# Performance work log

Measured on AMD Instinct MI355X. Metric: run time of the kernel, lower is better.

## Reference

```python
import jax, jax.numpy as jnp
import numpy as np

BL = 512  # block length (matches init bl)


def _conv1x1(w, b, x):
    # w: (out, in), b: (out,), x: (batch, in, L) -> (batch, out, L)
    return jnp.einsum('oi,bil->bol', w, x) + b[None, :, None]


def _window_mask(bl):
    # Faithful to torch loop: window_mask[:, :, i:i+bl] = 1 for i in range(bl)
    # -> all ones except the last column.
    wm = np.zeros((1, bl, bl + 2 * (bl // 2)), np.float32)
    for i in range(bl):
        wm[:, :, i:i + bl] = 1.0
    return jnp.asarray(wm)


def setup_inputs() -> dict:
    key = jax.random.key(0)
    ks = jax.random.split(key, 5)
    B, C, L = 1, 2048, 16384
    Cq = C // 2  # r1 = r2 = r3 = 2
    s_in = 1.0 / float(np.sqrt(C))
    s_mid = 1.0 / float(np.sqrt(Cq))
    return {
        'x1': jax.random.normal(ks[0], (B, C, L), jnp.float32),
        'x2': jnp.zeros((B, C, L), jnp.float32),
        'mask': jnp.ones((B, 1, L), jnp.float32),
        'wq': jax.random.normal(ks[1], (Cq, C), jnp.float32) * s_in,
        'bq': jnp.zeros((Cq,), jnp.float32),
        'wk': jax.random.normal(ks[2], (Cq, C), jnp.float32) * s_in,
        'bk': jnp.zeros((Cq,), jnp.float32),
        'wv': jax.random.normal(ks[3], (Cq, C), jnp.float32) * s_in,
        'bv': jnp.zeros((Cq,), jnp.float32),
        'wo': jax.random.normal(ks[4], (C, Cq), jnp.float32) * s_mid,
        'bo': jnp.zeros((C,), jnp.float32),
    }


def reference(x1, x2, mask, wq, bq, wk, bk, wv, bv, wo, bo):
    B, C, L = x1.shape  # B == 1 (asserted by sliding path)
    bl = BL
    nb = L // bl  # L % bl == 0 by construction
    half = bl // 2

    q = _conv1x1(wq, bq, x1)  # (1, c, L)
    k = _conv1x1(wk, bk, x1)
    v = _conv1x1(wv, bv, x1)  # encoder stage: value from x1 (x2 unused)
    c = q.shape[1]

    # query blocks: (nb, c, bl)
    qb = q.reshape(B, c, nb, bl).transpose(0, 2, 1, 3).reshape(nb, c, bl)

    # pad k/v/padding_mask with bl//2 zeros on both sides, then take overlapping
    # windows of width 2*bl per block.
    kp = jnp.pad(k, ((0, 0), (0, 0), (half, half)))[0]            # (c, L+bl)
    vp = jnp.pad(v, ((0, 0), (0, 0), (half, half)))[0]
    pm = jnp.pad(mask[:, 0:1, :], ((0, 0), (0, 0), (half, half)))[0]  # (1, L+bl)
    cols = np.arange(nb)[:, None] * bl + np.arange(2 * bl)[None, :]   # (nb, 2bl)
    kb = kp[:, cols].transpose(1, 0, 2)   # (nb, c, 2bl)
    vb = vp[:, cols].transpose(1, 0, 2)   # (nb, c, 2bl)
    pmb = pm[:, cols].transpose(1, 0, 2)  # (nb, 1, 2bl)

    final_mask = _window_mask(bl) * pmb   # (nb, bl, 2bl)

    # scalar dot attention with log-mask (as in AttentionHelper.scalar_dot_att)
    energy = jnp.einsum('ncl,ncm->nlm', qb, kb) / jnp.float32(np.sqrt(c))
    attn = jax.nn.softmax(energy + jnp.log(final_mask + 1e-9), axis=-1)
    attn = attn * final_mask
    out = jnp.einsum('ncm,nlm->ncl', vb, attn)  # (nb, c, bl)

    out = _conv1x1(wo, bo, jax.nn.relu(out))    # (nb, C, bl)
    out = out.reshape(B, nb, C, bl).transpose(0, 2, 1, 3).reshape(B, C, nb * bl)
    out = out[:, :, :L]
    return out * mask[:, 0:1, :]
```

## Files before the change

kernel.cpp:

```cpp
#include <hip/hip_runtime.h>
#include <hip/hip_bf16.h>

typedef __attribute__((ext_vector_type(4))) float f32x4;
typedef __attribute__((ext_vector_type(8))) __bf16 bf16x8;

struct ushort4_t { unsigned short x, y, z, w; };

#define DEVINL static __device__ __forceinline__

DEVINL unsigned short f2bf(float f) {
  union { float f; unsigned u; } x; x.f = f;
  return (unsigned short)((x.u + 0x7FFFu + ((x.u >> 16) & 1u)) >> 16);
}

DEVINL void gload16(const void* g, void* l) {
  __builtin_amdgcn_global_load_lds((const __attribute__((address_space(1))) void*)g,
                                   (__attribute__((address_space(3))) void*)l,
                                   16, 0, 0);
}

#define SBAR()   asm volatile("s_barrier" ::: "memory")
#define LGKM(n)  asm volatile("s_waitcnt lgkmcnt(" #n ")" ::: "memory")
#define VM(n)    asm volatile("s_waitcnt vmcnt(" #n ")" ::: "memory")
#define SCHED0() __builtin_amdgcn_sched_barrier(0)

__global__ __launch_bounds__(256) void transpose_x_k(const float* __restrict__ x,
                                                     unsigned short* __restrict__ xT) {
  __shared__ float tile[32][33];
  const int bx = blockIdx.x;
  const int by = blockIdx.y;
  const int tx = threadIdx.x;
  const int ty = threadIdx.y;
#pragma unroll
  for (int i = 0; i < 4; ++i) {
    int c = by * 32 + ty + i * 8;
    tile[ty + i * 8][tx] = x[(long)c * 16384 + bx * 32 + tx];
  }
  __syncthreads();
  const int t = ty * 32 + tx;
  const int lrow = t >> 3;
  const int cq = (t & 7) << 2;
  ushort4_t o;
  o.x = f2bf(tile[cq + 0][lrow]);
  o.y = f2bf(tile[cq + 1][lrow]);
  o.z = f2bf(tile[cq + 2][lrow]);
  o.w = f2bf(tile[cq + 3][lrow]);
  *reinterpret_cast<ushort4_t*>(xT + (long)(bx * 32 + lrow) * 2048 + by * 32 + cq) = o;
}

__global__ __launch_bounds__(256) void conv_w_k(const float* __restrict__ wq,
                                                const float* __restrict__ wk,
                                                const float* __restrict__ wv,
                                                const float* __restrict__ wo,
                                                unsigned short* __restrict__ Wqk,
                                                unsigned short* __restrict__ Wv,
                                                unsigned short* __restrict__ Wo) {
  long i = ((long)blockIdx.x * 256 + threadIdx.x) * 4;
  const float* src;
  unsigned short* dst;
  if (i < 4194304) {
    src = (i < 2097152) ? (wq + i) : (wk + i - 2097152);
    dst = Wqk + i;
  } else if (i < 6291456) {
    src = wv + (i - 4194304);
    dst = Wv + (i - 4194304);
  } else {
    src = wo + (i - 6291456);
    dst = Wo + (i - 6291456);
  }
  float4 v = *reinterpret_cast<const float4*>(src);
  ushort4_t o{f2bf(v.x), f2bf(v.y), f2bf(v.z), f2bf(v.w)};
  *reinterpret_cast<ushort4_t*>(dst) = o;
}

enum { EPI_QK = 0, EPI_V = 1, EPI_S = 2, EPI_PV = 3, EPI_OUT = 4 };

struct GArgs {
  const unsigned short* A;
  const unsigned short* Bt;
  void* C;
  const float* bias;
  const float* bias2;
  const float* mask;
  const unsigned short* guard;
  int aBatch, cBatch;
  int btRow0, btRow0Step, btRowLim;
  int btK0, btK0Step, btKLim;
};

template <int EPI, int GUARDED, int LDA, int LDB, int LDC, int KK>
__global__ __launch_bounds__(512, 2) void gemm8_k(GArgs g) {
  constexpr int NK = KK >> 6;
  __shared__ char lds[131072];

  const int t = threadIdx.x;
  const int l = t & 63;
  const int w = t >> 6;

  const int gx = gridDim.x, gxy = gx * gridDim.y;
  const int nwg = gxy * gridDim.z;
  int lin = blockIdx.z * gxy + blockIdx.y * gx + blockIdx.x;
  lin = (lin & 7) * (nwg >> 3) + (lin >> 3);
  const int z = lin / gxy;
  const int rres = lin - z * gxy;
  const int Mbase = (rres / gx) << 8;
  const int Nbase = (rres - (rres / gx) * gx) << 8;

  const int wr = w >> 2;
  const int wc = w & 3;
  const int fr = l & 15;
  const int fg = l >> 4;

  const unsigned short* Ab = g.A + (long)z * g.aBatch + (long)Mbase * LDA;
  const int bRowBase = g.btRow0 + z * g.btRow0Step + Nbase;
  const int bK0 = g.btK0 + z * g.btK0Step;

  const int rr = t >> 3;
  const int cb8s = t & 7;

  auto stage = [&](int bufSel, int unit, int kt) {
    const int k0 = (kt & (NK - 1)) << 6;
    const bool isA = (unit == 0) || (unit == 3);
#pragma unroll
    for (int gph = 0; gph < 2; ++gph) {
      int row;
      if (isA) row = (unit == 0 ? 0 : 64) + (gph << 7) + rr;
      else     row = (unit == 1 ? 0 : 32) + (gph << 7) + (rr & 31) + ((rr >> 5) << 6);
      const int cbL = cb8s ^ (row & 7);
      const int gk = k0 + (cbL << 3);
      char* lp = lds + (bufSel << 16) + (isA ? 0 : 32768) + row * 128 + (cb8s << 4);
      const char* gp;
      if (isA) {
        gp = (const char*)(Ab + (long)row * LDA + gk);
      } else if (!GUARDED) {
        gp = (const char*)(g.Bt + (long)(bRowBase + row) * LDB + (bK0 + gk));
      } else {
        const int grow = bRowBase + row;
        const int gkk = bK0 + gk;
        if ((unsigned)grow < (unsigned)g.btRowLim && (unsigned)gkk < (unsigned)g.btKLim)
          gp = (const char*)(g.Bt + (long)grow * LDB + gkk);
        else
          gp = (const char*)g.guard + (l << 4);
      }
      gload16(gp, lp);
    }
  };

  const int arow = (wr << 7) + fr;
  const int brow = (wc << 6) + fr;

  auto ldA = [&](int i8, int kk, int bufSel) -> bf16x8 {
    const int row = arow + (i8 << 4);
    const int cb = ((kk << 2) | fg) ^ (row & 7);
    return *(const bf16x8*)(lds + (bufSel << 16) + row * 128 + (cb << 4));
  };
  auto ldB = [&](int j, int kk, int bufSel) -> bf16x8 {
    const int row = brow + (j << 4);
    const int cb = ((kk << 2) | fg) ^ (row & 7);
    return *(const bf16x8*)(lds + (bufSel << 16) + 32768 + row * 128 + (cb << 4));
  };

  f32x4 acc[8][4];
#pragma unroll
  for (int i = 0; i < 8; ++i)
#pragma unroll
    for (int j = 0; j < 4; ++j) acc[i][j] = f32x4{0.f, 0.f, 0.f, 0.f};

  bf16x8 fa[4][2], fb[4][2];

#define MFMA_Q(QI, QJ)                                                        \
  __builtin_amdgcn_s_setprio(1);                                              \
  _Pragma("unroll") for (int kk = 0; kk < 2; ++kk)                            \
  _Pragma("unroll") for (int i = 0; i < 4; ++i)                               \
  _Pragma("unroll") for (int j = 0; j < 2; ++j)                               \
    acc[(QI)*4 + i][(QJ)*2 + j] = __builtin_amdgcn_mfma_f32_16x16x32_bf16(    \
        fa[i][kk], fb[(QJ)*2 + j][kk], acc[(QI)*4 + i][(QJ)*2 + j], 0, 0, 0); \
  __builtin_amdgcn_s_setprio(0);

  stage(0, 0, 0); stage(0, 1, 0); stage(0, 2, 0); stage(0, 3, 0);
  stage(1, 0, 1); stage(1, 1, 1); stage(1, 2, 1); stage(1, 3, 1);
  VM(8);
  SBAR();

#pragma unroll 1
  for (int kt = 0; kt < NK; ++kt) {
    const int cur = kt & 1;
    const int ktn = kt + 2;
#pragma unroll
    for (int i = 0; i < 4; ++i) { fa[i][0] = ldA(i, 0, cur); fa[i][1] = ldA(i, 1, cur); }
#pragma unroll
    for (int j = 0; j < 2; ++j) { fb[j][0] = ldB(j, 0, cur); fb[j][1] = ldB(j, 1, cur); }
    SCHED0();
#pragma unroll
    for (int j = 2; j < 4; ++j) { fb[j][0] = ldB(j, 0, cur); fb[j][1] = ldB(j, 1, cur); }
    LGKM(4); SCHED0();
    MFMA_Q(0, 0);
    SBAR();
    stage(cur, 0, ktn); stage(cur, 1, ktn);
    LGKM(0); SCHED0();
    MFMA_Q(0, 1);
#pragma unroll
    for (int i = 0; i < 4; ++i) { fa[i][0] = ldA(4 + i, 0, cur); fa[i][1] = ldA(4 + i, 1, cur); }
    LGKM(0); SCHED0();
    MFMA_Q(1, 0);
    SBAR();
    stage(cur, 2, ktn); stage(cur, 3, ktn);
    MFMA_Q(1, 1);
    VM(8); SBAR();
  }
  VM(0); LGKM(0); SBAR();

#pragma unroll
  for (int ii = 0; ii < 8; ++ii)
#pragma unroll
    for (int j = 0; j < 4; ++j)
#pragma unroll
      for (int r = 0; r < 4; ++r) {
        const int row = Mbase + (wr << 7) + ii * 16 + fg * 4 + r;
        const int col = Nbase + (wc << 6) + j * 16 + fr;
        float val = acc[ii][j][r];
        const long off = (long)z * g.cBatch + (long)row * LDC + col;
        if (EPI == EPI_QK) {
          val = (col < 1024) ? (val + g.bias[col]) * 0.03125f
                             : (val + g.bias2[col - 1024]);
          ((unsigned short*)g.C)[off] = f2bf(val);
        } else if (EPI == EPI_V) {
          val += g.bias[row];
          ((unsigned short*)g.C)[off] = f2bf(val);
        } else if (EPI == EPI_S) {
          ((float*)g.C)[off] = val;
        } else if (EPI == EPI_PV) {
          val = fmaxf(val, 0.f);
          ((unsigned short*)g.C)[off] = f2bf(val);
        } else {
          val = (val + g.bias[row]) * g.mask[col];
          ((float*)g.C)[off] = val;
        }
      }
#undef MFMA_Q
}

__global__ __launch_bounds__(256) void softmax_k(const float* __restrict__ S,
                                                 const float* __restrict__ mask,
                                                 unsigned short* __restrict__ P) {
  const int row = blockIdx.x;
  const int n = row >> 9;
  const float* s = S + (long)row * 1024;
  unsigned short* p = P + (long)row * 1024;
  const int t = threadIdx.x;

  const float4 sv = *reinterpret_cast<const float4*>(s + t * 4);
  const int pos0 = (n << 9) + t * 4 - 256;
  float4 mv = {0.f, 0.f, 0.f, 0.f};
  if ((unsigned)pos0 < 16384u) mv = *reinterpret_cast<const float4*>(mask + pos0);
  float fm[4] = {mv.x, mv.y, mv.z, mv.w};
  if (t == 255) fm[3] = 0.f;
  const float sc[4] = {sv.x, sv.y, sv.z, sv.w};

  float logit[4];
  float lmax = -3.0e38f;
#pragma unroll
  for (int k = 0; k < 4; ++k) {
    logit[k] = sc[k] + logf(fm[k] + 1e-9f);
    lmax = fmaxf(lmax, logit[k]);
  }
#pragma unroll
  for (int o = 32; o; o >>= 1) lmax = fmaxf(lmax, __shfl_xor(lmax, o, 64));
  __shared__ float red[8];
  const int wv_ = t >> 6, ln = t & 63;
  if (ln == 0) red[wv_] = lmax;
  __syncthreads();
  const float gmax = fmaxf(fmaxf(red[0], red[1]), fmaxf(red[2], red[3]));

  float e[4], lsum = 0.f;
#pragma unroll
  for (int k = 0; k < 4; ++k) { e[k] = expf(logit[k] - gmax); lsum += e[k]; }
#pragma unroll
  for (int o = 32; o; o >>= 1) lsum += __shfl_xor(lsum, o, 64);
  if (ln == 0) red[4 + wv_] = lsum;
  __syncthreads();
  const float inv = 1.f / ((red[4] + red[5]) + (red[6] + red[7]));
  ushort4_t o4;
  o4.x = f2bf(e[0] * inv * fm[0]);
  o4.y = f2bf(e[1] * inv * fm[1]);
  o4.z = f2bf(e[2] * inv * fm[2]);
  o4.w = f2bf(e[3] * inv * fm[3]);
  *reinterpret_cast<ushort4_t*>(p + t * 4) = o4;
}

extern "C" void kernel_launch(void* const* d_in, const int* in_sizes, int n_in,
                              void* d_out, int out_size, void* d_ws, size_t ws_size,
                              hipStream_t stream) {
  const float* x1 = (const float*)d_in[0];
  const float* mask = (const float*)d_in[2];
  const float* wq = (const float*)d_in[3];
  const float* bq = (const float*)d_in[4];
  const float* wk = (const float*)d_in[5];
  const float* bk = (const float*)d_in[6];
  const float* wv = (const float*)d_in[7];
  const float* bv = (const float*)d_in[8];
  const float* wo = (const float*)d_in[9];
  const float* bo = (const float*)d_in[10];

  char* ws = (char*)d_ws;
  unsigned short* xT   = (unsigned short*)(ws);
  unsigned short* attT = xT;
  unsigned short* Wqk  = (unsigned short*)(ws + 67108864);
  unsigned short* Wv   = (unsigned short*)(ws + 75497472);
  unsigned short* Wo   = (unsigned short*)(ws + 79691776);
  unsigned short* qkT  = (unsigned short*)(ws + 83886080);
  unsigned short* vbuf = (unsigned short*)(ws + 150994944);
  float*          Sbuf = (float*)(ws + 184549376);
  unsigned short* P    = (unsigned short*)(ws + 251658240);
  unsigned short* guard= (unsigned short*)(ws + 285212672);

  hipMemsetAsync(guard, 0, 4096, stream);

  transpose_x_k<<<dim3(512, 64), dim3(32, 8), 0, stream>>>(x1, xT);
  conv_w_k<<<dim3(8192), dim3(256), 0, stream>>>(wq, wk, wv, wo, Wqk, Wv, Wo);

  const int BIG = 0x40000000;
  {
    GArgs a{};
    a.A = xT; a.Bt = Wqk; a.C = qkT;
    a.bias = bq; a.bias2 = bk; a.guard = guard;
    a.aBatch = 0; a.cBatch = 0;
    a.btRow0 = 0; a.btRow0Step = 0; a.btRowLim = BIG;
    a.btK0 = 0; a.btK0Step = 0; a.btKLim = BIG;
    gemm8_k<EPI_QK, 0, 2048, 2048, 2048, 2048><<<dim3(8, 64, 1), 512, 0, stream>>>(a);
  }
  {
    GArgs a{};
    a.A = Wv; a.Bt = xT; a.C = vbuf;
    a.bias = bv; a.guard = guard;
    a.aBatch = 0; a.cBatch = 0;
    a.btRow0 = 0; a.btRow0Step = 0; a.btRowLim = BIG;
    a.btK0 = 0; a.btK0Step = 0; a.btKLim = BIG;
    gemm8_k<EPI_V, 0, 2048, 2048, 16384, 2048><<<dim3(64, 4, 1), 512, 0, stream>>>(a);
  }
  {
    GArgs a{};
    a.A = qkT; a.Bt = qkT; a.C = Sbuf;
    a.guard = guard;
    a.aBatch = 512 * 2048; a.cBatch = 512 * 1024;
    a.btRow0 = -256; a.btRow0Step = 512; a.btRowLim = 16384;
    a.btK0 = 1024; a.btK0Step = 0; a.btKLim = BIG;
    gemm8_k<EPI_S, 1, 2048, 2048, 1024, 1024><<<dim3(4, 2, 32), 512, 0, stream>>>(a);
  }
  softmax_k<<<dim3(16384), dim3(256), 0, stream>>>(Sbuf, mask, P);
  {
    GArgs a{};
    a.A = P; a.Bt = vbuf; a.C = attT;
    a.guard = guard;
    a.aBatch = 512 * 1024; a.cBatch = 512 * 1024;
    a.btRow0 = 0; a.btRow0Step = 0; a.btRowLim = BIG;
    a.btK0 = -256; a.btK0Step = 512; a.btKLim = 16384;
    gemm8_k<EPI_PV, 1, 1024, 16384, 1024, 1024><<<dim3(4, 2, 32), 512, 0, stream>>>(a);
  }
  {
    GArgs a{};
    a.A = Wo; a.Bt = attT; a.C = d_out;
    a.bias = bo; a.mask = mask; a.guard = guard;
    a.aBatch = 0; a.cBatch = 0;
    a.btRow0 = 0; a.btRow0Step = 0; a.btRowLim = BIG;
    a.btK0 = 0; a.btK0Step = 0; a.btKLim = BIG;
    gemm8_k<EPI_OUT, 0, 1024, 1024, 16384, 1024><<<dim3(64, 8, 1), 512, 0, stream>>>(a);
  }
  (void)in_sizes; (void)n_in; (void)out_size; (void)ws_size;
}
```

Baseline: 467.0 us.

## Load GEMM B operand directly from global into registers, halve LDS

The GEMM kernel no longer stages the B tile through LDS. Each wave reads its B fragments straight from global memory into registers, double-buffered in register sets (even/odd) one k-tile ahead, while A keeps its LDS double buffer, now at half the LDS size. The aim is to cut LDS traffic and LDS footprint and to simplify the pipeline. The cost is that the four row-waves load the same B data redundantly from global/L2, with less coalesced 16-byte per-lane reads and higher register pressure.

```diff
diff --git a/kernel.cpp b/kernel.cpp
--- a/kernel.cpp
+++ b/kernel.cpp
@@ -20,7 +20,7 @@
 }
 
 #define SBAR()   asm volatile("s_barrier" ::: "memory")
-#define LGKM(n)  asm volatile("s_waitcnt lgkmcnt(" #n ")" ::: "memory")
+#define LGKM0()  asm volatile("s_waitcnt lgkmcnt(0)" ::: "memory")
 #define VM(n)    asm volatile("s_waitcnt vmcnt(" #n ")" ::: "memory")
 #define SCHED0() __builtin_amdgcn_sched_barrier(0)
 
@@ -89,9 +89,9 @@
 };
 
 template <int EPI, int GUARDED, int LDA, int LDB, int LDC, int KK>
-__global__ __launch_bounds__(512, 2) void gemm8_k(GArgs g) {
+__global__ __launch_bounds__(512, 2) void gemmD_k(GArgs g) {
   constexpr int NK = KK >> 6;
-  __shared__ char lds[131072];
+  __shared__ char lds[65536];
 
   const int t = threadIdx.x;
   const int l = t & 63;
@@ -118,31 +118,15 @@
   const int rr = t >> 3;
   const int cb8s = t & 7;
 
-  auto stage = [&](int bufSel, int unit, int kt) {
+  auto stageA = [&](int bufSel, int half, int kt) {
     const int k0 = (kt & (NK - 1)) << 6;
-    const bool isA = (unit == 0) || (unit == 3);
 #pragma unroll
     for (int gph = 0; gph < 2; ++gph) {
-      int row;
-      if (isA) row = (unit == 0 ? 0 : 64) + (gph << 7) + rr;
-      else     row = (unit == 1 ? 0 : 32) + (gph << 7) + (rr & 31) + ((rr >> 5) << 6);
+      const int row = (half << 6) + (gph << 7) + rr;
       const int cbL = cb8s ^ (row & 7);
       const int gk = k0 + (cbL << 3);
-      char* lp = lds + (bufSel << 16) + (isA ? 0 : 32768) + row * 128 + (cb8s << 4);
-      const char* gp;
-      if (isA) {
-        gp = (const char*)(Ab + (long)row * LDA + gk);
-      } else if (!GUARDED) {
-        gp = (const char*)(g.Bt + (long)(bRowBase + row) * LDB + (bK0 + gk));
-      } else {
-        const int grow = bRowBase + row;
-        const int gkk = bK0 + gk;
-        if ((unsigned)grow < (unsigned)g.btRowLim && (unsigned)gkk < (unsigned)g.btKLim)
-          gp = (const char*)(g.Bt + (long)grow * LDB + gkk);
-        else
-          gp = (const char*)g.guard + (l << 4);
-      }
-      gload16(gp, lp);
+      char* lp = lds + (bufSel << 15) + row * 128 + (cb8s << 4);
+      gload16((const char*)(Ab + (long)row * LDA + gk), lp);
     }
   };
 
@@ -152,12 +136,20 @@
   auto ldA = [&](int i8, int kk, int bufSel) -> bf16x8 {
     const int row = arow + (i8 << 4);
     const int cb = ((kk << 2) | fg) ^ (row & 7);
-    return *(const bf16x8*)(lds + (bufSel << 16) + row * 128 + (cb << 4));
+    return *(const bf16x8*)(lds + (bufSel << 15) + row * 128 + (cb << 4));
   };
-  auto ldB = [&](int j, int kk, int bufSel) -> bf16x8 {
-    const int row = brow + (j << 4);
-    const int cb = ((kk << 2) | fg) ^ (row & 7);
-    return *(const bf16x8*)(lds + (bufSel << 16) + 32768 + row * 128 + (cb << 4));
+
+  auto ldBg = [&](int j, int kk, int kt) -> bf16x8 {
+    const int k0 = (kt & (NK - 1)) << 6;
+    const int gr = bRowBase + brow + (j << 4);
+    const int gc = bK0 + k0 + (kk << 5) + (fg << 3);
+    const unsigned short* ptr;
+    if (!GUARDED ||
+        ((unsigned)gr < (unsigned)g.btRowLim && (unsigned)gc < (unsigned)g.btKLim))
+      ptr = g.Bt + (long)gr * LDB + gc;
+    else
+      ptr = g.guard + ((l & 31) << 3);
+    return *(const bf16x8*)ptr;
   };
 
   f32x4 acc[8][4];
@@ -166,49 +158,46 @@
 #pragma unroll
     for (int j = 0; j < 4; ++j) acc[i][j] = f32x4{0.f, 0.f, 0.f, 0.f};
 
-  bf16x8 fa[4][2], fb[4][2];
-
-#define MFMA_Q(QI, QJ)                                                        \
+  bf16x8 fa[8][2], fbE[4][2], fbO[4][2];
+
+#define MQ2(I0, FB)                                                           \
   __builtin_amdgcn_s_setprio(1);                                              \
   _Pragma("unroll") for (int kk = 0; kk < 2; ++kk)                            \
   _Pragma("unroll") for (int i = 0; i < 4; ++i)                               \
-  _Pragma("unroll") for (int j = 0; j < 2; ++j)                               \
-    acc[(QI)*4 + i][(QJ)*2 + j] = __builtin_amdgcn_mfma_f32_16x16x32_bf16(    \
-        fa[i][kk], fb[(QJ)*2 + j][kk], acc[(QI)*4 + i][(QJ)*2 + j], 0, 0, 0); \
+  _Pragma("unroll") for (int j = 0; j < 4; ++j)                               \
+    acc[(I0) + i][j] = __builtin_amdgcn_mfma_f32_16x16x32_bf16(               \
+        fa[(I0) + i][kk], FB[j][kk], acc[(I0) + i][j], 0, 0, 0);              \
   __builtin_amdgcn_s_setprio(0);
 
-  stage(0, 0, 0); stage(0, 1, 0); stage(0, 2, 0); stage(0, 3, 0);
-  stage(1, 0, 1); stage(1, 1, 1); stage(1, 2, 1); stage(1, 3, 1);
-  VM(8);
+#define TILE(CUR, FBC, FBN, KT)                                               \
+  {                                                                           \
+    _Pragma("unroll") for (int i = 0; i < 8; ++i) {                           \
+      fa[i][0] = ldA(i, 0, CUR); fa[i][1] = ldA(i, 1, CUR); }                 \
+    _Pragma("unroll") for (int j = 0; j < 4; ++j) {                           \
+      FBN[j][0] = ldBg(j, 0, (KT) + 1); FBN[j][1] = ldBg(j, 1, (KT) + 1); }   \
+    MQ2(0, FBC);                                                              \
+    LGKM0(); SCHED0();                                                        \
+    SBAR();                                                                   \
+    stageA(CUR, 0, (KT) + 2); stageA(CUR, 1, (KT) + 2);                       \
+    MQ2(4, FBC);                                                              \
+    VM(12); SCHED0(); SBAR();                                                 \
+  }
+
+  stageA(0, 0, 0); stageA(0, 1, 0);
+  stageA(1, 0, 1); stageA(1, 1, 1);
+  SCHED0();
+#pragma unroll
+  for (int j = 0; j < 4; ++j) { fbE[j][0] = ldBg(j, 0, 0); fbE[j][1] = ldBg(j, 1, 0); }
+  SCHED0();
+  VM(12);
   SBAR();
 
 #pragma unroll 1
-  for (int kt = 0; kt < NK; ++kt) {
-    const int cur = kt & 1;
-    const int ktn = kt + 2;
-#pragma unroll
-    for (int i = 0; i < 4; ++i) { fa[i][0] = ldA(i, 0, cur); fa[i][1] = ldA(i, 1, cur); }
-#pragma unroll
-    for (int j = 0; j < 2; ++j) { fb[j][0] = ldB(j, 0, cur); fb[j][1] = ldB(j, 1, cur); }
-    SCHED0();
-#pragma unroll
-    for (int j = 2; j < 4; ++j) { fb[j][0] = ldB(j, 0, cur); fb[j][1] = ldB(j, 1, cur); }
-    LGKM(4); SCHED0();
-    MFMA_Q(0, 0);
-    SBAR();
-    stage(cur, 0, ktn); stage(cur, 1, ktn);
-    LGKM(0); SCHED0();
-    MFMA_Q(0, 1);
-#pragma unroll
-    for (int i = 0; i < 4; ++i) { fa[i][0] = ldA(4 + i, 0, cur); fa[i][1] = ldA(4 + i, 1, cur); }
-    LGKM(0); SCHED0();
-    MFMA_Q(1, 0);
-    SBAR();
-    stage(cur, 2, ktn); stage(cur, 3, ktn);
-    MFMA_Q(1, 1);
-    VM(8); SBAR();
-  }
-  VM(0); LGKM(0); SBAR();
+  for (int it = 0; it < NK / 2; ++it) {
+    TILE(0, fbE, fbO, 2 * it);
+    TILE(1, fbO, fbE, 2 * it + 1);
+  }
+  VM(0); LGKM0(); SBAR();
 
 #pragma unroll
   for (int ii = 0; ii < 8; ++ii)
@@ -237,7 +226,8 @@
           ((float*)g.C)[off] = val;
         }
       }
-#undef MFMA_Q
+#undef TILE
+#undef MQ2
 }
 
 __global__ __launch_bounds__(256) void softmax_k(const float* __restrict__ S,
@@ -327,7 +317,7 @@
     a.aBatch = 0; a.cBatch = 0;
     a.btRow0 = 0; a.btRow0Step = 0; a.btRowLim = BIG;
     a.btK0 = 0; a.btK0Step = 0; a.btKLim = BIG;
-    gemm8_k<EPI_QK, 0, 2048, 2048, 2048, 2048><<<dim3(8, 64, 1), 512, 0, stream>>>(a);
+    gemmD_k<EPI_QK, 0, 2048, 2048, 2048, 2048><<<dim3(8, 64, 1), 512, 0, stream>>>(a);
   }
   {
     GArgs a{};
@@ -336,7 +326,7 @@
     a.aBatch = 0; a.cBatch = 0;
     a.btRow0 = 0; a.btRow0Step = 0; a.btRowLim = BIG;
     a.btK0 = 0; a.btK0Step = 0; a.btKLim = BIG;
-    gemm8_k<EPI_V, 0, 2048, 2048, 16384, 2048><<<dim3(64, 4, 1), 512, 0, stream>>>(a);
+    gemmD_k<EPI_V, 0, 2048, 2048, 16384, 2048><<<dim3(64, 4, 1), 512, 0, stream>>>(a);
   }
   {
     GArgs a{};
@@ -345,7 +335,7 @@
     a.aBatch = 512 * 2048; a.cBatch = 512 * 1024;
     a.btRow0 = -256; a.btRow0Step = 512; a.btRowLim = 16384;
     a.btK0 = 1024; a.btK0Step = 0; a.btKLim = BIG;
-    gemm8_k<EPI_S, 1, 2048, 2048, 1024, 1024><<<dim3(4, 2, 32), 512, 0, stream>>>(a);
+    gemmD_k<EPI_S, 1, 2048, 2048, 1024, 1024><<<dim3(4, 2, 32), 512, 0, stream>>>(a);
   }
   softmax_k<<<dim3(16384), dim3(256), 0, stream>>>(Sbuf, mask, P);
   {
@@ -355,7 +345,7 @@
     a.aBatch = 512 * 1024; a.cBatch = 512 * 1024;
     a.btRow0 = 0; a.btRow0Step = 0; a.btRowLim = BIG;
     a.btK0 = -256; a.btK0Step = 512; a.btKLim = 16384;
-    gemm8_k<EPI_PV, 1, 1024, 16384, 1024, 1024><<<dim3(4, 2, 32), 512, 0, stream>>>(a);
+    gemmD_k<EPI_PV, 1, 1024, 16384, 1024, 1024><<<dim3(4, 2, 32), 512, 0, stream>>>(a);
   }
   {
     GArgs a{};
@@ -364,7 +354,7 @@
     a.aBatch = 0; a.cBatch = 0;
     a.btRow0 = 0; a.btRow0Step = 0; a.btRowLim = BIG;
     a.btK0 = 0; a.btK0Step = 0; a.btKLim = BIG;
-    gemm8_k<EPI_OUT, 0, 1024, 1024, 16384, 1024><<<dim3(64, 8, 1), 512, 0, stream>>>(a);
+    gemmD_k<EPI_OUT, 0, 1024, 1024, 16384, 1024><<<dim3(64, 8, 1), 512, 0, stream>>>(a);
   }
   (void)in_sizes; (void)n_in; (void)out_size; (void)ws_size;
 }
```

New measurement: 1.175 ms. +151.6%, slower.
